# Optimization experiments

Hardware: AMD Instinct MI355X
Metric: run time of the kernel (lower is better)

The kernel has to match this reference:

```python
import jax, jax.numpy as jnp
import numpy as np

B, CIN, HW = 32, 64, 56
K, KS, STRIDE, PAD = 128, 3, 1, 1


def setup_inputs() -> dict:
    key = jax.random.key(0)
    kx, kw, kb = jax.random.split(key, 3)
    x = jax.random.normal(kx, (B, CIN, HW, HW), dtype=jnp.float32)
    weight = jax.random.normal(kw, (K, CIN, KS, KS), dtype=jnp.float32)
    offset = jax.random.normal(kb, (K, 1, 1), dtype=jnp.float32)
    return {"x": x, "weight": weight, "offset": offset}


def reference(x, weight, offset):
    # conv2d (NCHW, OIHW) with stride/padding, then add per-kernel scalar offset.
    # Equivalent to the module's im2col (create_window_column_matrix) + matmul
    # + reshape, plus self.offset broadcast over (B, K, s, s).
    out = jax.lax.conv_general_dilated(
        x, weight,
        window_strides=(STRIDE, STRIDE),
        padding=[(PAD, PAD), (PAD, PAD)],
        dimension_numbers=("NCHW", "OIHW", "NCHW"),
    )
    return out + offset  # offset (K,1,1) broadcasts against (B,K,s,s)
```

## Files before the change

### kernel.cpp

```cpp
#include <hip/hip_runtime.h>
#include <hip/hip_bf16.h>

namespace {

using frag_t    = __attribute__((ext_vector_type(8))) short;
using f32x4     = __attribute__((ext_vector_type(4))) float;
using float4_t  = __attribute__((ext_vector_type(4))) float;

constexpr int BATCH = 32;
constexpr int CIN   = 64;
constexpr int HWD   = 56;
constexpr int KOUT  = 128;
constexpr int SP    = HWD * HWD;
constexpr int KD    = 9 * CIN;
constexpr int BN    = 128;
constexpr int HALO  = 57;
constexpr int NEXT  = BN + 2 * HALO;
constexpr int NTILES= SP / BN + 1;
constexpr int NWG2  = NTILES * BATCH * 2;
constexpr int TT    = BATCH * (SP / 64);
constexpr int WB    = (KOUT * KD + 255) / 256;

__device__ inline unsigned short f2bf(float f) {
    __hip_bfloat16 h = __float2bfloat16(f);
    return __builtin_bit_cast(unsigned short, h);
}

__global__ __launch_bounds__(256)
void prep_kernel(const float* __restrict__ x, const float* __restrict__ w,
                 unsigned short* __restrict__ wpA, unsigned short* __restrict__ xT)
{
    if (blockIdx.x >= TT) {
        const int idx = (blockIdx.x - TT) * 256 + threadIdx.x;
        if (idx < KOUT * KD) {
            const int kout = idx / KD, kk = idx - kout * KD;
            const int kc = kk >> 5, e = kk & 31;
            const int t = kk >> 6, c = kk & 63;
            const int ky = t / 3, kx = t - ky * 3;
            wpA[(kc * KOUT + kout) * 32 + e] = f2bf(w[((kout * CIN + c) * 3 + ky) * 3 + kx]);
        }
        return;
    }
    __shared__ float ls[64][68];
    const int bb   = blockIdx.x / (SP / 64);
    const int tile = blockIdx.x - bb * (SP / 64);
    const int sp0  = tile * 64;
    const int tid  = threadIdx.x;
    const int cq   = tid >> 4;
    const int spo  = (tid & 15) * 4;
    const float* xb = x + (size_t)bb * CIN * SP;
    #pragma unroll
    for (int j = 0; j < 4; ++j) {
        const int c = cq + 16 * j;
        float4_t v = *(const float4_t*)&xb[(size_t)c * SP + sp0 + spo];
        ls[spo + 0][c] = v.x; ls[spo + 1][c] = v.y;
        ls[spo + 2][c] = v.z; ls[spo + 3][c] = v.w;
    }
    __syncthreads();
    unsigned short* xo = xT + (size_t)(bb * SP + sp0) * 64;
    #pragma unroll
    for (int j = 0; j < 2; ++j) {
        const int s  = tid + 256 * j;
        const int sp = s >> 3, e = s & 7;
        frag_t u;
        #pragma unroll
        for (int q = 0; q < 8; ++q)
            u[q] = (short)f2bf(ls[sp][e * 8 + q]);
        *(frag_t*)&xo[sp * 64 + e * 8] = u;
    }
}

__global__ __launch_bounds__(256, 4)
void conv_mfma(const unsigned short* __restrict__ xT, const unsigned short* __restrict__ wpA,
               const float* __restrict__ off, float* __restrict__ out)
{
    __shared__ unsigned short xs[NEXT * 64];

    const int d    = blockIdx.x;
    const int wk   = (d & 7) * (NWG2 / 8) + (d >> 3);
    const int kh   = wk & 1;
    const int wk2  = wk >> 1;
    const int b    = wk2 / NTILES;
    const int sp0  = (wk2 - b * NTILES) * BN;
    const int tid  = threadIdx.x;
    const int lane = tid & 63;
    const int wid  = tid >> 6;

    {
        const unsigned short* xb = xT + (size_t)b * SP * 64;
        const int lsw = ((lane & 7) * 8) ^ ((lane >> 3) << 3);
        #pragma unroll
        for (int it = 0; it < 8; ++it) {
            const int R0 = it * 32 + wid * 8;
            const int r  = R0 + (lane >> 3);
            if (r < NEXT) {
                int g = sp0 - HALO + r;
                g = min(max(g, 0), SP - 1);
                const unsigned short* src = xb + (size_t)g * 64 + lsw;
                __builtin_amdgcn_global_load_lds(
                    (const __attribute__((address_space(1))) unsigned int*)src,
                    (__attribute__((address_space(3))) unsigned int*)&xs[R0 * 64 + (lane) * 8],
                    16, 0, 0);
            }
        }
    }
    asm volatile("s_waitcnt vmcnt(0)" ::: "memory");
    __syncthreads();

    const int wmL = (wid >> 1) * 32;
    const int wn  = (wid & 1) * 64;
    const int l15 = lane & 15;
    const int l4  = lane >> 4;

    unsigned long long mbits = 0ull;
    #pragma unroll
    for (int t = 0; t < 9; ++t) {
        const int dy = t / 3 - 1, dx = t % 3 - 1;
        #pragma unroll
        for (int nf = 0; nf < 4; ++nf) {
            const int sp = sp0 + wn + nf * 16 + l15;
            const int y  = sp / HWD;
            const int xc = sp - y * HWD;
            const bool v = ((unsigned)(y + dy) < (unsigned)HWD) &
                           ((unsigned)(xc + dx) < (unsigned)HWD);
            mbits |= (unsigned long long)(v ? 1 : 0) << (t * 4 + nf);
        }
    }

    const unsigned short* abase = wpA + (size_t)(kh * 64 + wmL + l15) * 32 + 8 * l4;
    const int cread = 8 * l4;
    const frag_t zf = {0,0,0,0,0,0,0,0};

    f32x4 acc[2][4] = {};

    #pragma unroll
    for (int kc = 0; kc < 18; ++kc) {
        const int t  = kc >> 1;
        const int c0 = (kc & 1) * 32;
        const int s    = (t / 3 - 1) * HWD + (t % 3 - 1);
        const int row0 = wn + l15 + HALO + s;
        const int sw   = (row0 & 7) << 3;
        frag_t a[2], bfr[4];
        #pragma unroll
        for (int mi = 0; mi < 2; ++mi)
            a[mi] = *(const frag_t*)(abase + (size_t)(kc * KOUT + mi * 16) * 32);
        #pragma unroll
        for (int nf = 0; nf < 4; ++nf) {
            const frag_t bl = *(const frag_t*)&xs[(row0 + 16 * nf) * 64
                                                 + ((c0 + cread) ^ sw)];
            bfr[nf] = ((mbits >> (t * 4 + nf)) & 1) ? bl : zf;
        }
        #pragma unroll
        for (int mi = 0; mi < 2; ++mi)
            #pragma unroll
            for (int nf = 0; nf < 4; ++nf)
                acc[mi][nf] = __builtin_amdgcn_mfma_f32_16x16x32_bf16(
                    a[mi], bfr[nf], acc[mi][nf], 0, 0, 0);
    }

    const int spn = sp0 + wn + l15;
    #pragma unroll
    for (int mi = 0; mi < 2; ++mi) {
        const int km = kh * 64 + wmL + 16 * mi + 4 * l4;
        #pragma unroll
        for (int reg = 0; reg < 4; ++reg) {
            const int  kk  = km + reg;
            const float ofv = off[kk];
            float* ob = out + (size_t)(b * KOUT + kk) * SP;
            #pragma unroll
            for (int nf = 0; nf < 4; ++nf) {
                const int sp = spn + 16 * nf;
                if (sp < SP) ob[sp] = acc[mi][nf][reg] + ofv;
            }
        }
    }
}

__global__ __launch_bounds__(256)
void conv3x3_kernel(const float* __restrict__ x, const float* __restrict__ w,
                    const float* __restrict__ off, float* __restrict__ out)
{
    const int s  = blockIdx.x * 256 + threadIdx.x;
    const int b  = s / SP;
    const int sp = s - b * SP;
    const int y  = sp / HWD;
    const int xx = sp - y * HWD;
    const int k0 = blockIdx.y * 4;

    const int   xm1 = (xx > 0) ? xx - 1 : 0;
    const int   xp1 = (xx < HWD - 1) ? xx + 1 : HWD - 1;
    const float m0  = (xx > 0) ? 1.f : 0.f;
    const float m2  = (xx < HWD - 1) ? 1.f : 0.f;

    int ro[3]; float msk[3][3];
    #pragma unroll
    for (int ky = 0; ky < 3; ++ky) {
        const int  yy = y + ky - 1;
        const bool ok = (unsigned)yy < (unsigned)HWD;
        const float rm = ok ? 1.f : 0.f;
        ro[ky] = (ok ? yy : 0) * HWD;
        msk[ky][0] = rm * m0; msk[ky][1] = rm; msk[ky][2] = rm * m2;
    }
    float acc[4] = {0.f, 0.f, 0.f, 0.f};
    const float* xb = x + (size_t)b * CIN * SP;
    for (int c = 0; c < CIN; ++c) {
        const float* xc = xb + (size_t)c * SP;
        #pragma unroll
        for (int ky = 0; ky < 3; ++ky) {
            const float* xr = xc + ro[ky];
            const float v0 = xr[xm1] * msk[ky][0];
            const float v1 = xr[xx]  * msk[ky][1];
            const float v2 = xr[xp1] * msk[ky][2];
            const int wi = c * 9 + ky * 3;
            #pragma unroll
            for (int kk = 0; kk < 4; ++kk) {
                const float* wr = w + (size_t)(k0 + kk) * (CIN * 9) + wi;
                acc[kk] = fmaf(v0, wr[0], acc[kk]);
                acc[kk] = fmaf(v1, wr[1], acc[kk]);
                acc[kk] = fmaf(v2, wr[2], acc[kk]);
            }
        }
    }
    #pragma unroll
    for (int kk = 0; kk < 4; ++kk)
        out[(size_t)(b * KOUT + k0 + kk) * SP + sp] = acc[kk] + off[k0 + kk];
}

}

extern "C" void kernel_launch(void* const* d_in, const int* in_sizes, int n_in,
                              void* d_out, int out_size, void* d_ws, size_t ws_size,
                              hipStream_t stream)
{
    const float* x   = (const float*)d_in[0];
    const float* w   = (const float*)d_in[1];
    const float* off = (const float*)d_in[2];
    float* out = (float*)d_out;

    const size_t wpa_bytes = (size_t)KOUT * KD * 2;
    const size_t xt_bytes  = (size_t)BATCH * SP * CIN * 2;

    if (ws_size >= wpa_bytes + xt_bytes) {
        unsigned short* wpA = (unsigned short*)d_ws;
        unsigned short* xT  = (unsigned short*)((char*)d_ws + wpa_bytes);
        prep_kernel<<<TT + WB, 256, 0, stream>>>(x, w, wpA, xT);
        conv_mfma<<<NWG2, dim3(256, 1, 1), 0, stream>>>(xT, wpA, off, out);
    } else {
        dim3 grid((BATCH * SP) / 256, KOUT / 4);
        conv3x3_kernel<<<grid, dim3(256, 1, 1), 0, stream>>>(x, w, off, out);
    }
}
```

Before: 43.72 us.

## Retile conv to 64-pixel tiles covering all 128 output channels per block

Each workgroup now computes all 128 output channels for a 64-pixel spatial tile, with each wave covering 32 channels. Before, two workgroups split the channels over a 128-pixel tile. The halo plus tile shrinks from 242 to 178 LDS rows, and the duplicate halo load for the two channel halves goes away. The LDS footprint drops, allowing 5 blocks per CU, and the ragged last-tile bounds check is removed because 3136 divides evenly by 64. The trade-off is a higher halo-to-tile ratio per pixel and fewer, lower-reuse B fragments per wave.

Result: faster. 42.34 us (-3.2%).

```diff
diff --git a/kernel.cpp b/kernel.cpp
--- a/kernel.cpp
+++ b/kernel.cpp
@@ -13,11 +13,12 @@
 constexpr int KOUT  = 128;
 constexpr int SP    = HWD * HWD;
 constexpr int KD    = 9 * CIN;
-constexpr int BN    = 128;
+constexpr int BN    = 64;
 constexpr int HALO  = 57;
-constexpr int NEXT  = BN + 2 * HALO;
-constexpr int NTILES= SP / BN + 1;
-constexpr int NWG2  = NTILES * BATCH * 2;
+constexpr int NROWS = BN + 2 * HALO;
+constexpr int NSTA  = 192;
+constexpr int NTILES= SP / BN;
+constexpr int NWG   = NTILES * BATCH;
 constexpr int TT    = BATCH * (SP / 64);
 constexpr int WB    = (KOUT * KD + 255) / 256;
 
@@ -70,18 +71,16 @@
     }
 }
 
-__global__ __launch_bounds__(256, 4)
-void conv_mfma(const unsigned short* __restrict__ xT, const unsigned short* __restrict__ wpA,
+__global__ __launch_bounds__(256, 5)
+void conv_slim(const unsigned short* __restrict__ xT, const unsigned short* __restrict__ wpA,
                const float* __restrict__ off, float* __restrict__ out)
 {
-    __shared__ unsigned short xs[NEXT * 64];
+    __shared__ unsigned short xs[NSTA * 64];
 
     const int d    = blockIdx.x;
-    const int wk   = (d & 7) * (NWG2 / 8) + (d >> 3);
-    const int kh   = wk & 1;
-    const int wk2  = wk >> 1;
-    const int b    = wk2 / NTILES;
-    const int sp0  = (wk2 - b * NTILES) * BN;
+    const int wk   = (d & 7) * (NWG / 8) + (d >> 3);
+    const int b    = wk / NTILES;
+    const int sp0  = (wk - b * NTILES) * BN;
     const int tid  = threadIdx.x;
     const int lane = tid & 63;
     const int wid  = tid >> 6;
@@ -90,16 +89,17 @@
         const unsigned short* xb = xT + (size_t)b * SP * 64;
         const int lsw = ((lane & 7) * 8) ^ ((lane >> 3) << 3);
         #pragma unroll
-        for (int it = 0; it < 8; ++it) {
+        for (int it = 0; it < 6; ++it) {
             const int R0 = it * 32 + wid * 8;
             const int r  = R0 + (lane >> 3);
-            if (r < NEXT) {
+            if (r < NROWS) {
                 int g = sp0 - HALO + r;
                 g = min(max(g, 0), SP - 1);
-                const unsigned short* src = xb + (size_t)g * 64 + lsw;
                 __builtin_amdgcn_global_load_lds(
-                    (const __attribute__((address_space(1))) unsigned int*)src,
-                    (__attribute__((address_space(3))) unsigned int*)&xs[R0 * 64 + (lane) * 8],
+                    (const __attribute__((address_space(1))) unsigned int*)
+                        (xb + (size_t)g * 64 + lsw),
+                    (__attribute__((address_space(3))) unsigned int*)
+                        &xs[R0 * 64 + lane * 8],
                     16, 0, 0);
             }
         }
@@ -107,27 +107,30 @@
     asm volatile("s_waitcnt vmcnt(0)" ::: "memory");
     __syncthreads();
 
-    const int wmL = (wid >> 1) * 32;
-    const int wn  = (wid & 1) * 64;
+    const int wm  = wid * 32;
     const int l15 = lane & 15;
     const int l4  = lane >> 4;
 
     unsigned long long mbits = 0ull;
+    int yv[4], xv[4];
+    #pragma unroll
+    for (int nf = 0; nf < 4; ++nf) {
+        const int sp = sp0 + nf * 16 + l15;
+        yv[nf] = sp / HWD;
+        xv[nf] = sp - yv[nf] * HWD;
+    }
     #pragma unroll
     for (int t = 0; t < 9; ++t) {
         const int dy = t / 3 - 1, dx = t % 3 - 1;
         #pragma unroll
         for (int nf = 0; nf < 4; ++nf) {
-            const int sp = sp0 + wn + nf * 16 + l15;
-            const int y  = sp / HWD;
-            const int xc = sp - y * HWD;
-            const bool v = ((unsigned)(y + dy) < (unsigned)HWD) &
-                           ((unsigned)(xc + dx) < (unsigned)HWD);
+            const bool v = ((unsigned)(yv[nf] + dy) < (unsigned)HWD) &
+                           ((unsigned)(xv[nf] + dx) < (unsigned)HWD);
             mbits |= (unsigned long long)(v ? 1 : 0) << (t * 4 + nf);
         }
     }
 
-    const unsigned short* abase = wpA + (size_t)(kh * 64 + wmL + l15) * 32 + 8 * l4;
+    const unsigned short* abase = wpA + (size_t)(wm + l15) * 32 + 8 * l4;
     const int cread = 8 * l4;
     const frag_t zf = {0,0,0,0,0,0,0,0};
 
@@ -138,7 +141,7 @@
         const int t  = kc >> 1;
         const int c0 = (kc & 1) * 32;
         const int s    = (t / 3 - 1) * HWD + (t % 3 - 1);
-        const int row0 = wn + l15 + HALO + s;
+        const int row0 = l15 + HALO + s;
         const int sw   = (row0 & 7) << 3;
         frag_t a[2], bfr[4];
         #pragma unroll
@@ -158,20 +161,18 @@
                     a[mi], bfr[nf], acc[mi][nf], 0, 0, 0);
     }
 
-    const int spn = sp0 + wn + l15;
+    const int spn = sp0 + l15;
     #pragma unroll
     for (int mi = 0; mi < 2; ++mi) {
-        const int km = kh * 64 + wmL + 16 * mi + 4 * l4;
+        const int km = wm + 16 * mi + 4 * l4;
         #pragma unroll
         for (int reg = 0; reg < 4; ++reg) {
             const int  kk  = km + reg;
             const float ofv = off[kk];
             float* ob = out + (size_t)(b * KOUT + kk) * SP;
             #pragma unroll
-            for (int nf = 0; nf < 4; ++nf) {
-                const int sp = spn + 16 * nf;
-                if (sp < SP) ob[sp] = acc[mi][nf][reg] + ofv;
-            }
+            for (int nf = 0; nf < 4; ++nf)
+                ob[spn + 16 * nf] = acc[mi][nf][reg] + ofv;
         }
     }
 }
@@ -244,7 +245,7 @@
         unsigned short* wpA = (unsigned short*)d_ws;
         unsigned short* xT  = (unsigned short*)((char*)d_ws + wpa_bytes);
         prep_kernel<<<TT + WB, 256, 0, stream>>>(x, w, wpA, xT);
-        conv_mfma<<<NWG2, dim3(256, 1, 1), 0, stream>>>(xT, wpA, off, out);
+        conv_slim<<<NWG, dim3(256, 1, 1), 0, stream>>>(xT, wpA, off, out);
     } else {
         dim3 grid((BATCH * SP) / 256, KOUT / 4);
         conv3x3_kernel<<<grid, dim3(256, 1, 1), 0, stream>>>(x, w, off, out);
```
